# Kernel tuning notes

Hardware: AMD Instinct MI355X
Metric: run time of the kernel (lower is better)

## Reference

```python
import jax, jax.numpy as jnp
import numpy as np

B, L, D = 1, 1024, 1024
NL = 4            # n_layers
N = 16            # d_state
DI = 2 * D        # d_inner (expand=2)
DTR = (D + 15) // 16  # dt_rank = ceil(d_model/16) = 64
K = 4             # depthwise conv kernel size
EPS = 1e-5


def setup_inputs() -> dict:
    key = jax.random.key(0)
    ks = jax.random.split(key, 8)
    s = lambda k, shp, sc: jax.random.normal(k, shp, jnp.float32) * sc
    x = s(ks[0], (B, L, D), 1.0)
    norm_w = jnp.ones((NL, D), jnp.float32)
    in_w = s(ks[1], (NL, 2 * DI, D), D ** -0.5)          # in_proj (no bias)
    conv_w = s(ks[2], (NL, DI, K), 0.5)                   # depthwise conv1d weight
    conv_b = s(ks[3], (NL, DI), 0.02)                     # conv1d bias
    xproj_w = s(ks[4], (NL, DTR + 2 * N, DI), DI ** -0.5) # x_proj (no bias)
    dt_w = s(ks[5], (NL, DI, DTR), DTR ** -0.5)           # dt_proj weight
    dt_b = jnp.full((NL, DI), 0.1, jnp.float32)           # dt_proj bias (positive-ish delta)
    A_log = jnp.log(jnp.tile(jnp.arange(1, N + 1, dtype=jnp.float32), (NL, DI, 1)))  # [NL, DI, N]
    D_skip = jnp.ones((NL, DI), jnp.float32)
    out_w = s(ks[6], (NL, D, DI), DI ** -0.5)             # out_proj (no bias)
    return dict(x=x, norm_w=norm_w, in_w=in_w, conv_w=conv_w, conv_b=conv_b,
                xproj_w=xproj_w, dt_w=dt_w, dt_b=dt_b, A_log=A_log,
                D_skip=D_skip, out_w=out_w)


def _rmsnorm(x, w):
    return x * jax.lax.rsqrt(jnp.mean(x * x, axis=-1, keepdims=True) + EPS) * w


def _causal_depthwise_conv(u, w, b):
    # u: [B, L, DI], w: [DI, K], b: [DI]; causal (left pad K-1)
    up = jnp.pad(u, ((0, 0), (K - 1, 0), (0, 0)))
    y = b
    for k in range(K):
        y = y + up[:, k:k + L, :] * w[:, k]
    return y


def _selective_scan(dA, dBu, C):
    # dA, dBu: [B, L, DI, N]; C: [B, L, N]
    def step(h, inp):
        a, bu, c = inp
        h = a * h + bu                       # [B, DI, N]
        y = jnp.einsum('bdn,bn->bd', h, c)   # [B, DI]
        return h, y
    h0 = jnp.zeros((dA.shape[0], DI, N), dA.dtype)
    _, ys = jax.lax.scan(step, h0, (dA.transpose(1, 0, 2, 3),
                                    dBu.transpose(1, 0, 2, 3),
                                    C.transpose(1, 0, 2)))
    return ys.transpose(1, 0, 2)             # [B, L, DI]


def _mamba_block(x, p):
    norm_w, in_w, conv_w, conv_b, xproj_w, dt_w, dt_b, A_log, D_skip, out_w = p
    xn = _rmsnorm(x, norm_w)
    xz = jnp.einsum('bld,ed->ble', xn, in_w)             # [B, L, 2*DI]
    u, z = jnp.split(xz, 2, axis=-1)
    u = jax.nn.silu(_causal_depthwise_conv(u, conv_w, conv_b))
    x_dbl = jnp.einsum('bld,ed->ble', u, xproj_w)        # [B, L, DTR+2N]
    dt_r, Bt, Ct = jnp.split(x_dbl, [DTR, DTR + N], axis=-1)
    delta = jax.nn.softplus(jnp.einsum('blr,dr->bld', dt_r, dt_w) + dt_b)  # [B, L, DI]
    A = -jnp.exp(A_log)                                  # [DI, N]
    dA = jnp.exp(delta[..., None] * A)                   # [B, L, DI, N]
    dBu = delta[..., None] * Bt[:, :, None, :] * u[..., None]
    y = _selective_scan(dA, dBu, Ct) + u * D_skip        # [B, L, DI]
    y = y * jax.nn.silu(z)
    return x + jnp.einsum('ble,de->bld', y, out_w)       # residual


def reference(x, norm_w, in_w, conv_w, conv_b, xproj_w, dt_w, dt_b, A_log, D_skip, out_w):
    params = (norm_w, in_w, conv_w, conv_b, xproj_w, dt_w, dt_b, A_log, D_skip, out_w)
    out, _ = jax.lax.scan(lambda h, p: (_mamba_block(h, p), None), x, params)
    return out
```

## Files before the change

### kernel.cpp

```cpp
#include <hip/hip_runtime.h>
#include <hip/hip_bf16.h>
#include <stdint.h>

#define L 1024
#define D 1024
#define NLAYER 4
#define NSTATE 16
#define DI 2048
#define DTR 64
#define KCONV 4
#define XD 96
#define NC 64
#define CT 16
#define KSPLIT 8

typedef __attribute__((ext_vector_type(8))) short short8;
typedef __attribute__((ext_vector_type(4))) float floatx4;

__device__ __forceinline__ float siluf(float x) { return x / (1.f + __expf(-x)); }

__device__ __forceinline__ unsigned int f2bf2(float lo, float hi) {
    __hip_bfloat16 a = __float2bfloat16(lo), b = __float2bfloat16(hi);
    return (unsigned int)*reinterpret_cast<unsigned short*>(&a) |
           ((unsigned int)*reinterpret_cast<unsigned short*>(&b) << 16);
}

#ifndef __has_builtin
#define __has_builtin(x) 0
#endif
#if __has_builtin(__builtin_amdgcn_global_load_lds)
#define HAVE_GLD 1
#define GLD(gp, lp) __builtin_amdgcn_global_load_lds(                                  \
    (const __attribute__((address_space(1))) void*)(gp),                               \
    (__attribute__((address_space(3))) void*)(lp), 16, 0, 0)
#endif

#define N_IN4  1048576
#define N_XP4  49152
#define N_DT4  32768
#define N_OUT4 524288
#define N_CVT4 (N_IN4 + N_XP4 + N_DT4 + N_OUT4)
#define CVT_THREADS (NLAYER * N_CVT4 / 4)

__global__ __launch_bounds__(256) void cvt_all_kernel(
    const float* __restrict__ in_w, const float* __restrict__ xp_w,
    const float* __restrict__ dt_w, const float* __restrict__ out_w,
    __hip_bfloat16* __restrict__ in_bf, __hip_bfloat16* __restrict__ xp_bf,
    __hip_bfloat16* __restrict__ dt_bf, __hip_bfloat16* __restrict__ out_bf) {
    int gi = blockIdx.x * 256 + threadIdx.x;
    if (gi >= CVT_THREADS) return;
    int layer = gi / (N_CVT4 / 4);
    int i = (gi - layer * (N_CVT4 / 4)) * 4;
    const float* src;
    __hip_bfloat16* dst;
    int off;
    if (i < N_IN4) {
        src = in_w + (size_t)layer * 4096 * 1024;
        dst = in_bf + (size_t)layer * 4096 * 1024; off = i;
    } else if (i < N_IN4 + N_XP4) {
        src = xp_w + (size_t)layer * 96 * 2048;
        dst = xp_bf + (size_t)layer * 128 * 2048; off = i - N_IN4;
    } else if (i < N_IN4 + N_XP4 + N_DT4) {
        src = dt_w + (size_t)layer * 2048 * 64;
        dst = dt_bf + (size_t)layer * 2048 * 64; off = i - N_IN4 - N_XP4;
    } else {
        src = out_w + (size_t)layer * 1024 * 2048;
        dst = out_bf + (size_t)layer * 1024 * 2048; off = i - N_IN4 - N_XP4 - N_DT4;
    }
    const float4* s4 = (const float4*)src + off;
    unsigned int o[8];
#pragma unroll
    for (int j = 0; j < 4; ++j) {
        float4 v = s4[j];
        o[j * 2 + 0] = f2bf2(v.x, v.y);
        o[j * 2 + 1] = f2bf2(v.z, v.w);
    }
    uint4* dp = (uint4*)((unsigned short*)dst + (size_t)off * 4);
    dp[0] = make_uint4(o[0], o[1], o[2], o[3]);
    dp[1] = make_uint4(o[4], o[5], o[6], o[7]);
}

__global__ __launch_bounds__(256) void rmsnorm_kernel(const float* __restrict__ x,
                                                      const float* __restrict__ w,
                                                      __hip_bfloat16* __restrict__ out) {
    int row = blockIdx.x;
    const float* xr = x + (size_t)row * D;
    float v[4];
    float s = 0.f;
#pragma unroll
    for (int i = 0; i < 4; ++i) {
        v[i] = xr[threadIdx.x + i * 256];
        s += v[i] * v[i];
    }
#pragma unroll
    for (int off = 32; off > 0; off >>= 1) s += __shfl_xor(s, off, 64);
    __shared__ float red[4];
    int wave = threadIdx.x >> 6;
    if ((threadIdx.x & 63) == 0) red[wave] = s;
    __syncthreads();
    float tot = red[0] + red[1] + red[2] + red[3];
    float inv = rsqrtf(tot * (1.f / D) + 1e-5f);
#pragma unroll
    for (int i = 0; i < 4; ++i) {
        int c = threadIdx.x + i * 256;
        out[(size_t)row * D + c] = __float2bfloat16(v[i] * inv * w[c]);
    }
}

#define BK 32

template <int TN, int EPI>
__global__ __launch_bounds__(256, 2) void gemm_mfma(
    const __hip_bfloat16* __restrict__ A, int lda,
    const __hip_bfloat16* __restrict__ B, int ldb,
    float* __restrict__ C, int ldc, int Nvalid,
    int kchunk, long zstride,
    const float* __restrict__ bias, const float* __restrict__ resid) {
    constexpr int NF = TN / 32;
    constexpr int WCOLS = TN / 2;
    __shared__ __align__(16) __hip_bfloat16 As[2][128 * BK];
    __shared__ __align__(16) __hip_bfloat16 Bs[2][TN * BK];
    int tid = threadIdx.x;
    int wave = tid >> 6, lane = tid & 63;
    int m0 = blockIdx.y * 128, n0 = blockIdx.x * TN;
    int k_lo = blockIdx.z * kchunk;
    int k_hi = k_lo + kchunk;
    C += (long)blockIdx.z * zstride;
    int wr = wave >> 1, wc = wave & 1;
    int srow = lane >> 2, scol = (lane & 3) * 8;
    int q = lane >> 4, r = lane & 15;

    floatx4 acc[4][NF] = {};

    const __hip_bfloat16* gA0 = A + (long)(m0 + wave * 32 + srow) * lda + scol;
    const __hip_bfloat16* gA1 = gA0 + (long)16 * lda;
    const __hip_bfloat16* gB0;
    const __hip_bfloat16* gB1 = nullptr;
    if (TN == 128) {
        gB0 = B + (long)(n0 + wave * 32 + srow) * ldb + scol;
        gB1 = gB0 + (long)16 * ldb;
    } else {
        gB0 = B + (long)(n0 + wave * 16 + srow) * ldb + scol;
    }

    auto stage = [&](int k0, int p) {
#ifdef HAVE_GLD
        GLD(gA0 + k0, &As[p][(wave * 32) * BK]);
        GLD(gA1 + k0, &As[p][(wave * 32 + 16) * BK]);
        GLD(gB0 + k0, &Bs[p][(wave * (TN == 128 ? 32 : 16)) * BK]);
        if (TN == 128) GLD(gB1 + k0, &Bs[p][(wave * 32 + 16) * BK]);
#else
        *(short8*)(&As[p][(wave * 32) * BK] + lane * 8) = *(const short8*)(gA0 + k0);
        *(short8*)(&As[p][(wave * 32 + 16) * BK] + lane * 8) = *(const short8*)(gA1 + k0);
        *(short8*)(&Bs[p][(wave * (TN == 128 ? 32 : 16)) * BK] + lane * 8) = *(const short8*)(gB0 + k0);
        if (TN == 128) *(short8*)(&Bs[p][(wave * 32 + 16) * BK] + lane * 8) = *(const short8*)(gB1 + k0);
#endif
    };

    stage(k_lo, 0);
    int p = 0;
    for (int k0 = k_lo; k0 < k_hi; k0 += BK) {
        __syncthreads();
        if (k0 + BK < k_hi) stage(k0 + BK, p ^ 1);
        const short* Ap = (const short*)As[p];
        const short* Bp = (const short*)Bs[p];
        short8 af[4], bfr[NF];
#pragma unroll
        for (int i = 0; i < 4; ++i)
            af[i] = *(const short8*)(Ap + (wr * 64 + i * 16 + r) * BK + q * 8);
#pragma unroll
        for (int j = 0; j < NF; ++j)
            bfr[j] = *(const short8*)(Bp + (wc * WCOLS + j * 16 + r) * BK + q * 8);
#pragma unroll
        for (int i = 0; i < 4; ++i)
#pragma unroll
            for (int j = 0; j < NF; ++j)
                acc[i][j] = __builtin_amdgcn_mfma_f32_16x16x32_bf16(af[i], bfr[j], acc[i][j], 0, 0, 0);
        p ^= 1;
    }

#pragma unroll
    for (int i = 0; i < 4; ++i) {
        int mrow = m0 + wr * 64 + i * 16 + q * 4;
#pragma unroll
        for (int j = 0; j < NF; ++j) {
            int ncol = n0 + wc * WCOLS + j * 16 + r;
            if (ncol < Nvalid) {
#pragma unroll
                for (int rr = 0; rr < 4; ++rr) {
                    float v = acc[i][j][rr];
                    int m = mrow + rr;
                    if (EPI == 1) {
                        v += bias[ncol];
                        v = v > 20.f ? v : log1pf(__expf(v));
                    } else if (EPI == 2) {
                        v += resid[(long)m * ldc + ncol];
                    }
                    C[(long)m * ldc + ncol] = v;
                }
            }
        }
    }
}

__global__ __launch_bounds__(256) void conv_silu_kernel(const float* __restrict__ xz,
                                                        const float* __restrict__ cw,
                                                        const float* __restrict__ cb,
                                                        __hip_bfloat16* __restrict__ u) {
    int idx = blockIdx.x * 256 + threadIdx.x;
    int d = idx & (DI - 1);
    int t = idx >> 11;
    float acc = cb[d];
#pragma unroll
    for (int k = 0; k < KCONV; ++k) {
        int tk = t - (KCONV - 1) + k;
        if (tk >= 0) acc += xz[(size_t)tk * (2 * DI) + d] * cw[d * KCONV + k];
    }
    u[idx] = __float2bfloat16(siluf(acc));
}

__global__ __launch_bounds__(256) void xdbl_reduce_kernel(const float* __restrict__ part,
                                                          float* __restrict__ xdbl,
                                                          __hip_bfloat16* __restrict__ xdbl_bf) {
    int i = blockIdx.x * 256 + threadIdx.x;
    float s = 0.f;
#pragma unroll
    for (int sp = 0; sp < KSPLIT; ++sp) s += part[(long)sp * L * XD + i];
    xdbl[i] = s;
    xdbl_bf[i] = __float2bfloat16(s);
}

__global__ __launch_bounds__(256) void scanA_kernel(const float* __restrict__ delta,
                                                    const __hip_bfloat16* __restrict__ u,
                                                    const float* __restrict__ xdbl,
                                                    const float* __restrict__ Alog,
                                                    float* __restrict__ Ach,
                                                    float* __restrict__ Bch) {
    int d = blockIdx.x * 256 + threadIdx.x;
    int c = blockIdx.y;
    __shared__ __align__(16) float Bsh[CT * NSTATE];
    int tt0 = threadIdx.x >> 4, c0 = threadIdx.x & 15;
    Bsh[threadIdx.x] = xdbl[(size_t)(c * CT + tt0) * XD + DTR + c0];
    __syncthreads();

    float aval[NSTATE];
    const float4* Al4 = (const float4*)(Alog + (size_t)d * NSTATE);
#pragma unroll
    for (int n4 = 0; n4 < 4; ++n4) {
        float4 t = Al4[n4];
        aval[n4 * 4 + 0] = -__expf(t.x);
        aval[n4 * 4 + 1] = -__expf(t.y);
        aval[n4 * 4 + 2] = -__expf(t.z);
        aval[n4 * 4 + 3] = -__expf(t.w);
    }
    float h[NSTATE], ap[NSTATE];
#pragma unroll
    for (int n = 0; n < NSTATE; ++n) { h[n] = 0.f; ap[n] = 1.f; }

    for (int tt = 0; tt < CT; ++tt) {
        int t = c * CT + tt;
        float dl = delta[(size_t)t * DI + d];
        float uu = __bfloat162float(u[(size_t)t * DI + d]);
        float du = dl * uu;
        const float4* Bv = (const float4*)(Bsh + tt * NSTATE);
#pragma unroll
        for (int n4 = 0; n4 < 4; ++n4) {
            float4 b = Bv[n4];
            float bb[4] = {b.x, b.y, b.z, b.w};
#pragma unroll
            for (int k = 0; k < 4; ++k) {
                int n = n4 * 4 + k;
                float a = __expf(dl * aval[n]);
                h[n] = a * h[n] + du * bb[k];
                ap[n] *= a;
            }
        }
    }
    float4* Ao = (float4*)(Ach + ((size_t)c * DI + d) * NSTATE);
    float4* Bo = (float4*)(Bch + ((size_t)c * DI + d) * NSTATE);
#pragma unroll
    for (int n4 = 0; n4 < 4; ++n4) {
        Ao[n4] = make_float4(ap[n4 * 4], ap[n4 * 4 + 1], ap[n4 * 4 + 2], ap[n4 * 4 + 3]);
        Bo[n4] = make_float4(h[n4 * 4], h[n4 * 4 + 1], h[n4 * 4 + 2], h[n4 * 4 + 3]);
    }
}

__global__ __launch_bounds__(256) void scanB_kernel(float* __restrict__ Ach,
                                                    const float* __restrict__ Bch) {
    long i = blockIdx.x * 256 + threadIdx.x;
    const long S = (long)DI * NSTATE;
    float h = 0.f;
    for (int c = 0; c < NC; ++c) {
        float a = Ach[c * S + i];
        float b = Bch[c * S + i];
        Ach[c * S + i] = h;
        h = a * h + b;
    }
}

__global__ __launch_bounds__(256) void scanC_kernel(const float* __restrict__ delta,
                                                    const __hip_bfloat16* __restrict__ u,
                                                    const float* __restrict__ xdbl,
                                                    const float* __restrict__ Alog,
                                                    const float* __restrict__ Hin,
                                                    const float* __restrict__ xz,
                                                    const float* __restrict__ Dskip,
                                                    __hip_bfloat16* __restrict__ yg) {
    int d = blockIdx.x * 256 + threadIdx.x;
    int c = blockIdx.y;
    __shared__ __align__(16) float Bsh[CT * NSTATE];
    __shared__ __align__(16) float Csh[CT * NSTATE];
    int tt0 = threadIdx.x >> 4, c0 = threadIdx.x & 15;
    Bsh[threadIdx.x] = xdbl[(size_t)(c * CT + tt0) * XD + DTR + c0];
    Csh[threadIdx.x] = xdbl[(size_t)(c * CT + tt0) * XD + DTR + NSTATE + c0];
    __syncthreads();

    float aval[NSTATE];
    const float4* Al4 = (const float4*)(Alog + (size_t)d * NSTATE);
#pragma unroll
    for (int n4 = 0; n4 < 4; ++n4) {
        float4 t = Al4[n4];
        aval[n4 * 4 + 0] = -__expf(t.x);
        aval[n4 * 4 + 1] = -__expf(t.y);
        aval[n4 * 4 + 2] = -__expf(t.z);
        aval[n4 * 4 + 3] = -__expf(t.w);
    }
    float h[NSTATE];
    const float4* Hi = (const float4*)(Hin + ((size_t)c * DI + d) * NSTATE);
#pragma unroll
    for (int n4 = 0; n4 < 4; ++n4) {
        float4 t = Hi[n4];
        h[n4 * 4 + 0] = t.x; h[n4 * 4 + 1] = t.y; h[n4 * 4 + 2] = t.z; h[n4 * 4 + 3] = t.w;
    }
    float dsk = Dskip[d];

    for (int tt = 0; tt < CT; ++tt) {
        int t = c * CT + tt;
        float dl = delta[(size_t)t * DI + d];
        float uu = __bfloat162float(u[(size_t)t * DI + d]);
        float du = dl * uu;
        const float4* Bv = (const float4*)(Bsh + tt * NSTATE);
        const float4* Cv = (const float4*)(Csh + tt * NSTATE);
        float y = 0.f;
#pragma unroll
        for (int n4 = 0; n4 < 4; ++n4) {
            float4 b = Bv[n4];
            float4 cc = Cv[n4];
            float bb[4] = {b.x, b.y, b.z, b.w};
            float cv[4] = {cc.x, cc.y, cc.z, cc.w};
#pragma unroll
            for (int k = 0; k < 4; ++k) {
                int n = n4 * 4 + k;
                float a = __expf(dl * aval[n]);
                h[n] = a * h[n] + du * bb[k];
                y += h[n] * cv[k];
            }
        }
        float z = xz[(size_t)t * (2 * DI) + DI + d];
        yg[(size_t)t * DI + d] = __float2bfloat16((y + uu * dsk) * siluf(z));
    }
}

extern "C" void kernel_launch(void* const* d_in, const int* in_sizes, int n_in,
                              void* d_out, int out_size, void* d_ws, size_t ws_size,
                              hipStream_t stream) {
    const float* x      = (const float*)d_in[0];
    const float* norm_w = (const float*)d_in[1];
    const float* in_w   = (const float*)d_in[2];
    const float* conv_w = (const float*)d_in[3];
    const float* conv_b = (const float*)d_in[4];
    const float* xproj_w= (const float*)d_in[5];
    const float* dt_w   = (const float*)d_in[6];
    const float* dt_b   = (const float*)d_in[7];
    const float* A_log  = (const float*)d_in[8];
    const float* D_skip = (const float*)d_in[9];
    const float* out_w  = (const float*)d_in[10];
    float* out = (float*)d_out;

    uint8_t* wp = (uint8_t*)d_ws;
    auto alloc = [&](size_t bytes) {
        uint8_t* p = wp;
        wp += (bytes + 255) & ~(size_t)255;
        return p;
    };
    __hip_bfloat16* w_in_bf  = (__hip_bfloat16*)alloc((size_t)NLAYER * 4096 * 1024 * 2);
    __hip_bfloat16* w_xp_bf  = (__hip_bfloat16*)alloc((size_t)NLAYER * 128 * 2048 * 2);
    __hip_bfloat16* w_dt_bf  = (__hip_bfloat16*)alloc((size_t)NLAYER * 2048 * 64 * 2);
    __hip_bfloat16* w_out_bf = (__hip_bfloat16*)alloc((size_t)NLAYER * 1024 * 2048 * 2);
    __hip_bfloat16* xn_bf    = (__hip_bfloat16*)alloc((size_t)L * D * 2);
    float*          xz       = (float*)alloc((size_t)L * 2 * DI * 4);
    __hip_bfloat16* u_bf     = (__hip_bfloat16*)alloc((size_t)L * DI * 2);
    float*          xdbl     = (float*)alloc((size_t)L * XD * 4);
    __hip_bfloat16* xdbl_bf  = (__hip_bfloat16*)alloc((size_t)L * XD * 2);
    float*          part     = (float*)alloc((size_t)KSPLIT * L * XD * 4);
    float*          delta    = (float*)alloc((size_t)L * DI * 4);
    __hip_bfloat16* yg_bf    = (__hip_bfloat16*)alloc((size_t)L * DI * 2);
    float*          Ach      = (float*)alloc((size_t)NC * DI * NSTATE * 4);
    float*          Bch      = (float*)alloc((size_t)NC * DI * NSTATE * 4);

    cvt_all_kernel<<<(CVT_THREADS + 255) / 256, 256, 0, stream>>>(
        in_w, xproj_w, dt_w, out_w, w_in_bf, w_xp_bf, w_dt_bf, w_out_bf);

    for (int l = 0; l < NLAYER; ++l) {
        const float* xin = (l == 0) ? x : out;
        const __hip_bfloat16* wi = w_in_bf + (size_t)l * 4096 * 1024;
        const __hip_bfloat16* wx = w_xp_bf + (size_t)l * 128 * 2048;
        const __hip_bfloat16* wd = w_dt_bf + (size_t)l * 2048 * 64;
        const __hip_bfloat16* wo = w_out_bf + (size_t)l * 1024 * 2048;

        rmsnorm_kernel<<<L, 256, 0, stream>>>(xin, norm_w + (size_t)l * D, xn_bf);

        gemm_mfma<64, 0><<<dim3(4096 / 64, L / 128, 1), 256, 0, stream>>>(
            xn_bf, D, wi, D, xz, 4096, 4096, D, 0, nullptr, nullptr);

        conv_silu_kernel<<<L * DI / 256, 256, 0, stream>>>(
            xz, conv_w + (size_t)l * DI * KCONV, conv_b + (size_t)l * DI, u_bf);

        gemm_mfma<64, 0><<<dim3(2, L / 128, KSPLIT), 256, 0, stream>>>(
            u_bf, DI, wx, DI, part, XD, XD, DI / KSPLIT, (long)L * XD, nullptr, nullptr);
        xdbl_reduce_kernel<<<(L * XD) / 256, 256, 0, stream>>>(part, xdbl, xdbl_bf);

        gemm_mfma<64, 1><<<dim3(2048 / 64, L / 128, 1), 256, 0, stream>>>(
            xdbl_bf, XD, wd, DTR, delta, DI, DI, DTR, 0,
            dt_b + (size_t)l * DI, nullptr);

        scanA_kernel<<<dim3(DI / 256, NC), 256, 0, stream>>>(
            delta, u_bf, xdbl, A_log + (size_t)l * DI * NSTATE, Ach, Bch);
        scanB_kernel<<<(DI * NSTATE) / 256, 256, 0, stream>>>(Ach, Bch);
        scanC_kernel<<<dim3(DI / 256, NC), 256, 0, stream>>>(
            delta, u_bf, xdbl, A_log + (size_t)l * DI * NSTATE, Ach, xz,
            D_skip + (size_t)l * DI, yg_bf);

        gemm_mfma<64, 2><<<dim3(1024 / 64, L / 128, 1), 256, 0, stream>>>(
            yg_bf, DI, wo, DI, out, D, D, DI, 0, nullptr, xin);
    }
}
```

Baseline: 669.3 us.

## Fuse x_proj split-K reduction into consumers and split-K the out_proj GEMM

Removes the xdbl_reduce kernel. The dt_proj GEMM now sums the KSPLIT partial x_proj results while staging its A tile and converts them to bf16 itself, and scanA/scanC sum the B and C partials directly. The out_proj GEMM is split into two K halves, which doubles its grid from 128 blocks, and a new reduce2 kernel adds the halves and the residual. This trades one launch and some extra redundant partial reads for better occupancy on the out_proj GEMM, at the cost of an extra partial-buffer write and read plus a launch.

```diff
diff --git a/kernel.cpp b/kernel.cpp
--- a/kernel.cpp
+++ b/kernel.cpp
@@ -13,16 +13,25 @@
 #define NC 64
 #define CT 16
 #define KSPLIT 8
+#define BK 32
 
 typedef __attribute__((ext_vector_type(8))) short short8;
 typedef __attribute__((ext_vector_type(4))) float floatx4;
 
 __device__ __forceinline__ float siluf(float x) { return x / (1.f + __expf(-x)); }
 
-__device__ __forceinline__ unsigned int f2bf2(float lo, float hi) {
-    __hip_bfloat16 a = __float2bfloat16(lo), b = __float2bfloat16(hi);
-    return (unsigned int)*reinterpret_cast<unsigned short*>(&a) |
-           ((unsigned int)*reinterpret_cast<unsigned short*>(&b) << 16);
+__device__ __forceinline__ unsigned short f2bf(float x) {
+    __hip_bfloat16 b = __float2bfloat16(x);
+    return *reinterpret_cast<unsigned short*>(&b);
+}
+
+__device__ __forceinline__ short8 pack8(floatx4 a, floatx4 b) {
+    short8 o;
+    o[0] = (short)f2bf(a.x); o[1] = (short)f2bf(a.y);
+    o[2] = (short)f2bf(a.z); o[3] = (short)f2bf(a.w);
+    o[4] = (short)f2bf(b.x); o[5] = (short)f2bf(b.y);
+    o[6] = (short)f2bf(b.z); o[7] = (short)f2bf(b.w);
+    return o;
 }
 
 #ifndef __has_builtin
@@ -72,8 +81,8 @@
 #pragma unroll
     for (int j = 0; j < 4; ++j) {
         float4 v = s4[j];
-        o[j * 2 + 0] = f2bf2(v.x, v.y);
-        o[j * 2 + 1] = f2bf2(v.z, v.w);
+        o[j * 2 + 0] = (unsigned int)f2bf(v.x) | ((unsigned int)f2bf(v.y) << 16);
+        o[j * 2 + 1] = (unsigned int)f2bf(v.z) | ((unsigned int)f2bf(v.w) << 16);
     }
     uint4* dp = (uint4*)((unsigned short*)dst + (size_t)off * 4);
     dp[0] = make_uint4(o[0], o[1], o[2], o[3]);
@@ -107,53 +116,66 @@
     }
 }
 
-#define BK 32
-
-template <int TN, int EPI>
+template <int EPI, bool ARED>
 __global__ __launch_bounds__(256, 2) void gemm_mfma(
-    const __hip_bfloat16* __restrict__ A, int lda,
-    const __hip_bfloat16* __restrict__ B, int ldb,
+    const void* __restrict__ Ax, int lda,
+    const __hip_bfloat16* __restrict__ Bw, int ldb,
     float* __restrict__ C, int ldc, int Nvalid,
     int kchunk, long zstride,
-    const float* __restrict__ bias, const float* __restrict__ resid) {
-    constexpr int NF = TN / 32;
-    constexpr int WCOLS = TN / 2;
+    const float* __restrict__ bias, long pstride) {
     __shared__ __align__(16) __hip_bfloat16 As[2][128 * BK];
-    __shared__ __align__(16) __hip_bfloat16 Bs[2][TN * BK];
+    __shared__ __align__(16) __hip_bfloat16 Bs[2][64 * BK];
     int tid = threadIdx.x;
     int wave = tid >> 6, lane = tid & 63;
-    int m0 = blockIdx.y * 128, n0 = blockIdx.x * TN;
-    int k_lo = blockIdx.z * kchunk;
-    int k_hi = k_lo + kchunk;
+    int m0 = blockIdx.y * 128, n0 = blockIdx.x * 64;
+    int k_lo = blockIdx.z * kchunk, k_hi = k_lo + kchunk;
     C += (long)blockIdx.z * zstride;
     int wr = wave >> 1, wc = wave & 1;
     int srow = lane >> 2, scol = (lane & 3) * 8;
     int q = lane >> 4, r = lane & 15;
 
-    floatx4 acc[4][NF] = {};
-
-    const __hip_bfloat16* gA0 = A + (long)(m0 + wave * 32 + srow) * lda + scol;
-    const __hip_bfloat16* gA1 = gA0 + (long)16 * lda;
-    const __hip_bfloat16* gB0;
-    const __hip_bfloat16* gB1 = nullptr;
-    if (TN == 128) {
-        gB0 = B + (long)(n0 + wave * 32 + srow) * ldb + scol;
-        gB1 = gB0 + (long)16 * ldb;
+    floatx4 acc[4][2] = {};
+
+    const __hip_bfloat16* gA0b = nullptr;
+    const __hip_bfloat16* gA1b = nullptr;
+    const float* gA0f = nullptr;
+    const float* gA1f = nullptr;
+    if (!ARED) {
+        gA0b = (const __hip_bfloat16*)Ax + (long)(m0 + wave * 32 + srow) * lda + scol;
+        gA1b = gA0b + (long)16 * lda;
     } else {
-        gB0 = B + (long)(n0 + wave * 16 + srow) * ldb + scol;
-    }
+        gA0f = (const float*)Ax + (long)(m0 + wave * 32 + srow) * lda + scol;
+        gA1f = gA0f + (long)16 * lda;
+    }
+    const __hip_bfloat16* gB = Bw + (long)(n0 + wave * 16 + srow) * ldb + scol;
 
     auto stage = [&](int k0, int p) {
+        if (!ARED) {
 #ifdef HAVE_GLD
-        GLD(gA0 + k0, &As[p][(wave * 32) * BK]);
-        GLD(gA1 + k0, &As[p][(wave * 32 + 16) * BK]);
-        GLD(gB0 + k0, &Bs[p][(wave * (TN == 128 ? 32 : 16)) * BK]);
-        if (TN == 128) GLD(gB1 + k0, &Bs[p][(wave * 32 + 16) * BK]);
+            GLD(gA0b + k0, &As[p][(wave * 32) * BK]);
+            GLD(gA1b + k0, &As[p][(wave * 32 + 16) * BK]);
 #else
-        *(short8*)(&As[p][(wave * 32) * BK] + lane * 8) = *(const short8*)(gA0 + k0);
-        *(short8*)(&As[p][(wave * 32 + 16) * BK] + lane * 8) = *(const short8*)(gA1 + k0);
-        *(short8*)(&Bs[p][(wave * (TN == 128 ? 32 : 16)) * BK] + lane * 8) = *(const short8*)(gB0 + k0);
-        if (TN == 128) *(short8*)(&Bs[p][(wave * 32 + 16) * BK] + lane * 8) = *(const short8*)(gB1 + k0);
+            *(short8*)(&As[p][(wave * 32) * BK + lane * 8]) = *(const short8*)(gA0b + k0);
+            *(short8*)(&As[p][(wave * 32 + 16) * BK + lane * 8]) = *(const short8*)(gA1b + k0);
+#endif
+        } else {
+            floatx4 v0 = {0.f, 0.f, 0.f, 0.f}, v1 = v0, w0 = v0, w1 = v0;
+#pragma unroll
+            for (int sp = 0; sp < KSPLIT; ++sp) {
+                const float* p0 = gA0f + sp * pstride + k0;
+                const float* p1 = gA1f + sp * pstride + k0;
+                v0 += *(const floatx4*)(p0);
+                v1 += *(const floatx4*)(p0 + 4);
+                w0 += *(const floatx4*)(p1);
+                w1 += *(const floatx4*)(p1 + 4);
+            }
+            *(short8*)(&As[p][(wave * 32 + srow) * BK + scol]) = pack8(v0, v1);
+            *(short8*)(&As[p][(wave * 32 + 16 + srow) * BK + scol]) = pack8(w0, w1);
+        }
+#ifdef HAVE_GLD
+        GLD(gB + k0, &Bs[p][(wave * 16) * BK]);
+#else
+        *(short8*)(&Bs[p][(wave * 16) * BK + lane * 8]) = *(const short8*)(gB + k0);
 #endif
     };
 
@@ -164,17 +186,17 @@
         if (k0 + BK < k_hi) stage(k0 + BK, p ^ 1);
         const short* Ap = (const short*)As[p];
         const short* Bp = (const short*)Bs[p];
-        short8 af[4], bfr[NF];
+        short8 af[4], bfr[2];
 #pragma unroll
         for (int i = 0; i < 4; ++i)
             af[i] = *(const short8*)(Ap + (wr * 64 + i * 16 + r) * BK + q * 8);
 #pragma unroll
-        for (int j = 0; j < NF; ++j)
-            bfr[j] = *(const short8*)(Bp + (wc * WCOLS + j * 16 + r) * BK + q * 8);
+        for (int j = 0; j < 2; ++j)
+            bfr[j] = *(const short8*)(Bp + (wc * 32 + j * 16 + r) * BK + q * 8);
 #pragma unroll
         for (int i = 0; i < 4; ++i)
 #pragma unroll
-            for (int j = 0; j < NF; ++j)
+            for (int j = 0; j < 2; ++j)
                 acc[i][j] = __builtin_amdgcn_mfma_f32_16x16x32_bf16(af[i], bfr[j], acc[i][j], 0, 0, 0);
         p ^= 1;
     }
@@ -183,8 +205,8 @@
     for (int i = 0; i < 4; ++i) {
         int mrow = m0 + wr * 64 + i * 16 + q * 4;
 #pragma unroll
-        for (int j = 0; j < NF; ++j) {
-            int ncol = n0 + wc * WCOLS + j * 16 + r;
+        for (int j = 0; j < 2; ++j) {
+            int ncol = n0 + wc * 32 + j * 16 + r;
             if (ncol < Nvalid) {
 #pragma unroll
                 for (int rr = 0; rr < 4; ++rr) {
@@ -193,14 +215,23 @@
                     if (EPI == 1) {
                         v += bias[ncol];
                         v = v > 20.f ? v : log1pf(__expf(v));
-                    } else if (EPI == 2) {
-                        v += resid[(long)m * ldc + ncol];
                     }
                     C[(long)m * ldc + ncol] = v;
                 }
             }
         }
     }
+}
+
+__global__ __launch_bounds__(256) void reduce2_kernel(const float* __restrict__ part2,
+                                                      const float* __restrict__ xin,
+                                                      float* __restrict__ out) {
+    int i = blockIdx.x * 256 + threadIdx.x;
+    float4 a = ((const float4*)part2)[i];
+    float4 b = ((const float4*)(part2 + (size_t)L * D))[i];
+    float4 c = ((const float4*)xin)[i];
+    ((float4*)out)[i] = make_float4(a.x + b.x + c.x, a.y + b.y + c.y,
+                                    a.z + b.z + c.z, a.w + b.w + c.w);
 }
 
 __global__ __launch_bounds__(256) void conv_silu_kernel(const float* __restrict__ xz,
@@ -219,20 +250,9 @@
     u[idx] = __float2bfloat16(siluf(acc));
 }
 
-__global__ __launch_bounds__(256) void xdbl_reduce_kernel(const float* __restrict__ part,
-                                                          float* __restrict__ xdbl,
-                                                          __hip_bfloat16* __restrict__ xdbl_bf) {
-    int i = blockIdx.x * 256 + threadIdx.x;
-    float s = 0.f;
-#pragma unroll
-    for (int sp = 0; sp < KSPLIT; ++sp) s += part[(long)sp * L * XD + i];
-    xdbl[i] = s;
-    xdbl_bf[i] = __float2bfloat16(s);
-}
-
 __global__ __launch_bounds__(256) void scanA_kernel(const float* __restrict__ delta,
                                                     const __hip_bfloat16* __restrict__ u,
-                                                    const float* __restrict__ xdbl,
+                                                    const float* __restrict__ part,
                                                     const float* __restrict__ Alog,
                                                     float* __restrict__ Ach,
                                                     float* __restrict__ Bch) {
@@ -240,7 +260,13 @@
     int c = blockIdx.y;
     __shared__ __align__(16) float Bsh[CT * NSTATE];
     int tt0 = threadIdx.x >> 4, c0 = threadIdx.x & 15;
-    Bsh[threadIdx.x] = xdbl[(size_t)(c * CT + tt0) * XD + DTR + c0];
+    {
+        float s = 0.f;
+        size_t base = (size_t)(c * CT + tt0) * XD + DTR + c0;
+#pragma unroll
+        for (int sp = 0; sp < KSPLIT; ++sp) s += part[(size_t)sp * L * XD + base];
+        Bsh[threadIdx.x] = s;
+    }
     __syncthreads();
 
     float aval[NSTATE];
@@ -300,7 +326,7 @@
 
 __global__ __launch_bounds__(256) void scanC_kernel(const float* __restrict__ delta,
                                                     const __hip_bfloat16* __restrict__ u,
-                                                    const float* __restrict__ xdbl,
+                                                    const float* __restrict__ part,
                                                     const float* __restrict__ Alog,
                                                     const float* __restrict__ Hin,
                                                     const float* __restrict__ xz,
@@ -311,8 +337,17 @@
     __shared__ __align__(16) float Bsh[CT * NSTATE];
     __shared__ __align__(16) float Csh[CT * NSTATE];
     int tt0 = threadIdx.x >> 4, c0 = threadIdx.x & 15;
-    Bsh[threadIdx.x] = xdbl[(size_t)(c * CT + tt0) * XD + DTR + c0];
-    Csh[threadIdx.x] = xdbl[(size_t)(c * CT + tt0) * XD + DTR + NSTATE + c0];
+    {
+        float sb = 0.f, sc = 0.f;
+        size_t base = (size_t)(c * CT + tt0) * XD + DTR + c0;
+#pragma unroll
+        for (int sp = 0; sp < KSPLIT; ++sp) {
+            sb += part[(size_t)sp * L * XD + base];
+            sc += part[(size_t)sp * L * XD + base + NSTATE];
+        }
+        Bsh[threadIdx.x] = sb;
+        Csh[threadIdx.x] = sc;
+    }
     __syncthreads();
 
     float aval[NSTATE];
@@ -390,11 +425,10 @@
     __hip_bfloat16* xn_bf    = (__hip_bfloat16*)alloc((size_t)L * D * 2);
     float*          xz       = (float*)alloc((size_t)L * 2 * DI * 4);
     __hip_bfloat16* u_bf     = (__hip_bfloat16*)alloc((size_t)L * DI * 2);
-    float*          xdbl     = (float*)alloc((size_t)L * XD * 4);
-    __hip_bfloat16* xdbl_bf  = (__hip_bfloat16*)alloc((size_t)L * XD * 2);
     float*          part     = (float*)alloc((size_t)KSPLIT * L * XD * 4);
     float*          delta    = (float*)alloc((size_t)L * DI * 4);
     __hip_bfloat16* yg_bf    = (__hip_bfloat16*)alloc((size_t)L * DI * 2);
+    float*          part2    = (float*)alloc((size_t)2 * L * D * 4);
     float*          Ach      = (float*)alloc((size_t)NC * DI * NSTATE * 4);
     float*          Bch      = (float*)alloc((size_t)NC * DI * NSTATE * 4);
 
@@ -410,28 +444,28 @@
 
         rmsnorm_kernel<<<L, 256, 0, stream>>>(xin, norm_w + (size_t)l * D, xn_bf);
 
-        gemm_mfma<64, 0><<<dim3(4096 / 64, L / 128, 1), 256, 0, stream>>>(
-            xn_bf, D, wi, D, xz, 4096, 4096, D, 0, nullptr, nullptr);
+        gemm_mfma<0, false><<<dim3(4096 / 64, L / 128, 1), 256, 0, stream>>>(
+            xn_bf, D, wi, D, xz, 4096, 4096, D, 0, nullptr, 0);
 
         conv_silu_kernel<<<L * DI / 256, 256, 0, stream>>>(
             xz, conv_w + (size_t)l * DI * KCONV, conv_b + (size_t)l * DI, u_bf);
 
-        gemm_mfma<64, 0><<<dim3(2, L / 128, KSPLIT), 256, 0, stream>>>(
-            u_bf, DI, wx, DI, part, XD, XD, DI / KSPLIT, (long)L * XD, nullptr, nullptr);
-        xdbl_reduce_kernel<<<(L * XD) / 256, 256, 0, stream>>>(part, xdbl, xdbl_bf);
-
-        gemm_mfma<64, 1><<<dim3(2048 / 64, L / 128, 1), 256, 0, stream>>>(
-            xdbl_bf, XD, wd, DTR, delta, DI, DI, DTR, 0,
-            dt_b + (size_t)l * DI, nullptr);
+        gemm_mfma<0, false><<<dim3(2, L / 128, KSPLIT), 256, 0, stream>>>(
+            u_bf, DI, wx, DI, part, XD, XD, DI / KSPLIT, (long)L * XD, nullptr, 0);
+
+        gemm_mfma<1, true><<<dim3(2048 / 64, L / 128, 1), 256, 0, stream>>>(
+            part, XD, wd, DTR, delta, DI, DI, DTR, 0,
+            dt_b + (size_t)l * DI, (long)L * XD);
 
         scanA_kernel<<<dim3(DI / 256, NC), 256, 0, stream>>>(
-            delta, u_bf, xdbl, A_log + (size_t)l * DI * NSTATE, Ach, Bch);
+            delta, u_bf, part, A_log + (size_t)l * DI * NSTATE, Ach, Bch);
         scanB_kernel<<<(DI * NSTATE) / 256, 256, 0, stream>>>(Ach, Bch);
         scanC_kernel<<<dim3(DI / 256, NC), 256, 0, stream>>>(
-            delta, u_bf, xdbl, A_log + (size_t)l * DI * NSTATE, Ach, xz,
+            delta, u_bf, part, A_log + (size_t)l * DI * NSTATE, Ach, xz,
             D_skip + (size_t)l * DI, yg_bf);
 
-        gemm_mfma<64, 2><<<dim3(1024 / 64, L / 128, 1), 256, 0, stream>>>(
-            yg_bf, DI, wo, DI, out, D, D, DI, 0, nullptr, xin);
-    }
-}
+        gemm_mfma<0, false><<<dim3(1024 / 64, L / 128, 2), 256, 0, stream>>>(
+            yg_bf, DI, wo, DI, part2, D, D, DI / 2, (long)L * D, nullptr, 0);
+        reduce2_kernel<<<(L * D / 4) / 256, 256, 0, stream>>>(part2, xin, out);
+    }
+}
```

New measurement: 638.1 us. -4.7%, faster.
